# Optimization experiments

Measured on AMD Instinct MI355X. Metric: run time of the kernel, lower is better.

Reference implementation:

```python
import jax, jax.numpy as jnp
import numpy as np

B, C, W = 32, 128, 4096          # batch, channel (= emb_dim = D), window/input_dim
HID = [2048, 1024, 512]          # encoder hidden dims (last dim transforms)
K, D = 512, 128                  # codebook: K = hidden_dims[-1], D = emb_dim
BETA = 0.25


def setup_inputs() -> dict:
    key = jax.random.key(0)
    ks = jax.random.split(key, 12)
    def lin(k, fan_in, fan_out):
        return jax.random.normal(k, (fan_in, fan_out), jnp.float32) * (1.0 / np.sqrt(fan_in))
    inp = {"x": jax.random.normal(ks[0], (B, C, W), jnp.float32)}
    edims = [W] + HID  # 4096 -> 2048 -> 1024 -> 512
    for i in range(3):
        inp[f"ew{i}"] = lin(ks[1 + i], edims[i], edims[i + 1])
        inp[f"eb{i}"] = jnp.zeros((edims[i + 1],), jnp.float32)
    inp["codebook"] = jax.random.uniform(ks[4], (K, D), jnp.float32, -1.0 / K, 1.0 / K)
    ddims = [512, 1024, 2048, 4096]  # decoder mirrors encoder
    for i in range(3):
        inp[f"dw{i}"] = lin(ks[5 + i], ddims[i], ddims[i + 1])
        inp[f"db{i}"] = jnp.zeros((ddims[i + 1],), jnp.float32)
    return inp


def reference(x, ew0, eb0, ew1, eb1, ew2, eb2, codebook, dw0, db0, dw1, db1, dw2, db2):
    # ---- encoder: LinearBlock = Linear + ReLU over last dim ----
    h = x
    for wgt, b in ((ew0, eb0), (ew1, eb1), (ew2, eb2)):
        h = jax.nn.relu(h @ wgt + b)            # [B, C, L] with L shrinking to 512

    # ---- VectorQuantizer1d ----
    lat = jnp.swapaxes(h, 1, 2)                 # [B, L, D]
    flat = lat.reshape(-1, D)                   # [B*L, D]
    # cdist^2 via expansion, then argmin -> nearest-codebook lookup
    dist = (jnp.sum(flat * flat, axis=1, keepdims=True)
            + jnp.sum(codebook * codebook, axis=1)
            - 2.0 * flat @ codebook.T)          # [B*L, K]
    inds = jnp.argmin(dist, axis=1)             # [B*L]
    q = codebook[inds].reshape(lat.shape)       # one-hot matmul == gather

    commit = jnp.mean((jax.lax.stop_gradient(q) - lat) ** 2)
    embed = jnp.mean((q - jax.lax.stop_gradient(lat)) ** 2)
    vq_loss = BETA * commit + embed

    q_st = lat + jax.lax.stop_gradient(q - lat)  # straight-through estimator
    z = jnp.swapaxes(q_st, 1, 2)                 # back to [B, D, L]

    # ---- decoder: Linear+ReLU blocks, last block has no activation ----
    for i, (wgt, b) in enumerate(((dw0, db0), (dw1, db1), (dw2, db2))):
        z = z @ wgt + b
        if i < 2:
            z = jax.nn.relu(z)
    return z, x, vq_loss
```

## Files before the change

### kernel.cpp

```cpp
#include <hip/hip_runtime.h>


typedef _Float16 f16;
typedef _Float16 f16x8 __attribute__((ext_vector_type(8)));
typedef _Float16 f16x4 __attribute__((ext_vector_type(4)));
typedef float    f32x4 __attribute__((ext_vector_type(4)));

typedef const unsigned int __attribute__((address_space(1)))* gp1_t;
typedef unsigned int __attribute__((address_space(3)))*       lp3_t;

__device__ __forceinline__ void gl_lds16(const void* g, void* l) {
  __builtin_amdgcn_global_load_lds((gp1_t)g, (lp3_t)l, 16, 0, 0);
}

#define BATCH 32
#define CDIM  128
#define WDIM  4096
#define LDIM  512
#define KCB   512
#define DCB   128

#define SX    128.0f
#define SW    256.0f
#define SA    256.0f
#define SCB   4096.0f
#define SQ    4096.0f

#define BM 128
#define BN 128
#define BK 32

template<int SPLIT, int EPI>
__global__ __launch_bounds__(256, 2)
void vq_gemm(const f16* __restrict__ Ah, const f16* __restrict__ Al,
             const f16* __restrict__ Bh, const f16* __restrict__ Bl,
             const float* __restrict__ bias,
             void* __restrict__ Co, void* __restrict__ Co2,
             int M, int N, int K, float unscale, float outscale)
{
  __shared__ __align__(16) f16 sAh[BM * BK];
  __shared__ __align__(16) f16 sBh[BN * BK];
  __shared__ __align__(16) f16 sAl[SPLIT ? BM * BK : 8];
  __shared__ __align__(16) f16 sBl[SPLIT ? BN * BK : 8];

  const int tid  = threadIdx.x;
  const int lane = tid & 63;
  const int w    = tid >> 6;
  const int nb   = N / BN;
  const int bx   = blockIdx.x % nb;
  const int by   = blockIdx.x / nb;
  const int m0   = by * BM, n0 = bx * BN;
  const int wr   = w >> 1, wc = w & 1;
  const int fr   = lane & 15;
  const int ko   = (lane >> 4) * 8;

  f32x4 acc[4][4] = {};

  const int srow = lane >> 2;
  const int skb  = (lane & 3) * 8;

  for (int k0 = 0; k0 < K; k0 += BK) {
#pragma unroll
    for (int i = 0; i < 2; ++i) {
      const int c  = w * 2 + i;
      const size_t ga = (size_t)(m0 + c * 16 + srow) * K + k0 + skb;
      const size_t gb = (size_t)(n0 + c * 16 + srow) * K + k0 + skb;
      gl_lds16(Ah + ga, &sAh[c * 512]);
      gl_lds16(Bh + gb, &sBh[c * 512]);
      if (SPLIT) {
        gl_lds16(Al + ga, &sAl[c * 512]);
        gl_lds16(Bl + gb, &sBl[c * 512]);
      }
    }
    __syncthreads();

    f16x8 ah[4], bh[4], al[4], bl[4];
#pragma unroll
    for (int mi = 0; mi < 4; ++mi) {
      const int r = (wr * 64 + mi * 16 + fr) * BK + ko;
      ah[mi] = *(const f16x8*)&sAh[r];
      if (SPLIT) al[mi] = *(const f16x8*)&sAl[r];
    }
#pragma unroll
    for (int ni = 0; ni < 4; ++ni) {
      const int r = (wc * 64 + ni * 16 + fr) * BK + ko;
      bh[ni] = *(const f16x8*)&sBh[r];
      if (SPLIT) bl[ni] = *(const f16x8*)&sBl[r];
    }
#pragma unroll
    for (int mi = 0; mi < 4; ++mi)
#pragma unroll
      for (int ni = 0; ni < 4; ++ni) {
        acc[mi][ni] = __builtin_amdgcn_mfma_f32_16x16x32_f16(ah[mi], bh[ni], acc[mi][ni], 0, 0, 0);
        if (SPLIT) {
          acc[mi][ni] = __builtin_amdgcn_mfma_f32_16x16x32_f16(ah[mi], bl[ni], acc[mi][ni], 0, 0, 0);
          acc[mi][ni] = __builtin_amdgcn_mfma_f32_16x16x32_f16(al[mi], bh[ni], acc[mi][ni], 0, 0, 0);
        }
      }
    __syncthreads();
  }

  const int r4 = (lane >> 4) * 4;
#pragma unroll
  for (int mi = 0; mi < 4; ++mi) {
#pragma unroll
    for (int ni = 0; ni < 4; ++ni) {
      const int col = n0 + wc * 64 + ni * 16 + fr;
      const float bv = (EPI == 0) ? 0.0f : bias[col];
#pragma unroll
      for (int j = 0; j < 4; ++j) {
        const int row = m0 + wr * 64 + mi * 16 + r4 + j;
        float y = acc[mi][ni][j] * unscale;
        if (EPI != 0) y += bv;
        if (EPI == 1 || EPI == 2) y = fmaxf(y, 0.0f);
        const size_t idx = (size_t)row * N + col;
        if (EPI == 0 || EPI == 3) {
          ((float*)Co)[idx] = y;
        } else {
          const float ys = y * outscale;
          const f16 hi = (f16)ys;
          ((f16*)Co)[idx] = hi;
          if (EPI == 1) ((f16*)Co2)[idx] = (f16)(ys - (float)hi);
        }
      }
    }
  }
}

__global__ void vq_split(const float* __restrict__ in, f16* __restrict__ hi,
                         f16* __restrict__ lo, int n4, float scale)
{
  const int i = blockIdx.x * 256 + threadIdx.x;
  if (i >= n4) return;
  const float4 v = ((const float4*)in)[i];
  f16x4 h, l;
#pragma unroll
  for (int j = 0; j < 4; ++j) {
    const float s = (&v.x)[j] * scale;
    const f16 hh = (f16)s;
    h[j] = hh;
    l[j] = (f16)(s - (float)hh);
  }
  *(f16x4*)&hi[i * 4] = h;
  *(f16x4*)&lo[i * 4] = l;
}

template<int WRITE_LO>
__global__ void vq_tsplit(const float* __restrict__ W, f16* __restrict__ Th,
                          f16* __restrict__ Tl, int K, int N, float scale)
{
  __shared__ float t[32][33];
  const int n0 = blockIdx.x * 32, k0 = blockIdx.y * 32;
  const int tx = threadIdx.x & 31, ty = threadIdx.x >> 5;
#pragma unroll
  for (int i = 0; i < 4; ++i)
    t[ty + i * 8][tx] = W[(size_t)(k0 + ty + i * 8) * N + n0 + tx];
  __syncthreads();
#pragma unroll
  for (int i = 0; i < 4; ++i) {
    const int n = n0 + ty + i * 8;
    const float v = t[tx][ty + i * 8] * scale;
    const f16 hi = (f16)v;
    Th[(size_t)n * K + k0 + tx] = hi;
    if (WRITE_LO) Tl[(size_t)n * K + k0 + tx] = (f16)(v - (float)hi);
  }
}

__global__ void vq_tpose(const f16* __restrict__ Hh, const f16* __restrict__ Hl,
                         f16* __restrict__ Fh, f16* __restrict__ Fl)
{
  __shared__ f16 th[32][33];
  __shared__ f16 tl[32][33];
  const int bidx = blockIdx.x;
  const int b = bidx >> 6, rem = bidx & 63;
  const int l0 = (rem >> 2) * 32, c0 = (rem & 3) * 32;
  const int tx = threadIdx.x & 31, ty = threadIdx.x >> 5;
  const size_t hbase = (size_t)b * CDIM * LDIM;
#pragma unroll
  for (int i = 0; i < 4; ++i) {
    const int c = c0 + ty + i * 8;
    th[ty + i * 8][tx] = Hh[hbase + (size_t)c * LDIM + l0 + tx];
    tl[ty + i * 8][tx] = Hl[hbase + (size_t)c * LDIM + l0 + tx];
  }
  __syncthreads();
  const size_t fbase = (size_t)b * LDIM * DCB;
#pragma unroll
  for (int i = 0; i < 4; ++i) {
    const int l = l0 + ty + i * 8;
    Fh[fbase + (size_t)l * DCB + c0 + tx] = th[tx][ty + i * 8];
    Fl[fbase + (size_t)l * DCB + c0 + tx] = tl[tx][ty + i * 8];
  }
}

__global__ void vq_cbnorm(const float* __restrict__ cb, float* __restrict__ cbn)
{
  const int k = blockIdx.x * 256 + threadIdx.x;
  if (k >= KCB) return;
  float s = 0.f;
  for (int c = 0; c < DCB; ++c) { const float v = cb[k * DCB + c]; s += v * v; }
  cbn[k] = s;
}

__global__ void vq_argmin(const float* __restrict__ G, const float* __restrict__ cbn,
                          int* __restrict__ inds)
{
  const int row = blockIdx.x;
  const int lane = threadIdx.x;
  const float* g = G + (size_t)row * KCB;
  float best = 1e30f; int bi = 0;
#pragma unroll
  for (int j = 0; j < 8; ++j) {
    const int k = j * 64 + lane;
    const float d = cbn[k] - 2.0f * g[k];
    if (d < best) { best = d; bi = k; }
  }
  for (int off = 32; off; off >>= 1) {
    const float ov = __shfl_xor(best, off);
    const int oi = __shfl_xor(bi, off);
    if (ov < best || (ov == best && oi < bi)) { best = ov; bi = oi; }
  }
  if (lane == 0) inds[row] = bi;
}

__global__ void vq_gather(const float* __restrict__ cb, const int* __restrict__ inds,
                          f16* __restrict__ z0)
{
  const int t = blockIdx.x * 256 + threadIdx.x;
  const int l = t & 511, c = (t >> 9) & 127, b = t >> 16;
  const int ind = inds[b * LDIM + l];
  z0[t] = (f16)(cb[ind * DCB + c] * SQ);
}

__global__ void vq_loss(const f16* __restrict__ Fh, const f16* __restrict__ Fl,
                        const float* __restrict__ cb, const int* __restrict__ inds,
                        float* __restrict__ partials)
{
  const int gw = (blockIdx.x * 256 + threadIdx.x) >> 6;
  const int lane = threadIdx.x & 63;
  float s = 0.f;
  for (int r = gw; r < BATCH * LDIM; r += 1024) {
    const int ind = inds[r];
    const f16* fh = Fh + (size_t)r * DCB;
    const f16* fl = Fl + (size_t)r * DCB;
    const float* q = cb + (size_t)ind * DCB;
#pragma unroll
    for (int j = 0; j < 2; ++j) {
      const int c = j * 64 + lane;
      const float lat = ((float)fh[c] + (float)fl[c]) * (1.0f / SA);
      const float d = q[c] - lat;
      s += d * d;
    }
  }
  for (int off = 32; off; off >>= 1) s += __shfl_xor(s, off);
  __shared__ float wsum[4];
  if (lane == 0) wsum[threadIdx.x >> 6] = s;
  __syncthreads();
  if (threadIdx.x == 0) partials[blockIdx.x] = wsum[0] + wsum[1] + wsum[2] + wsum[3];
}

__global__ void vq_loss_final(const float* __restrict__ partials, float* __restrict__ out)
{
  float s = partials[threadIdx.x];
  for (int off = 32; off; off >>= 1) s += __shfl_xor(s, off);
  __shared__ float wsum[4];
  if ((threadIdx.x & 63) == 0) wsum[threadIdx.x >> 6] = s;
  __syncthreads();
  if (threadIdx.x == 0)
    out[0] = (wsum[0] + wsum[1] + wsum[2] + wsum[3]) * (1.25f / (float)(BATCH * LDIM * DCB));
}

extern "C" void kernel_launch(void* const* d_in, const int* in_sizes, int n_in,
                              void* d_out, int out_size, void* d_ws, size_t ws_size,
                              hipStream_t stream)
{
  const float* x   = (const float*)d_in[0];
  const float* ew0 = (const float*)d_in[1];
  const float* eb0 = (const float*)d_in[2];
  const float* ew1 = (const float*)d_in[3];
  const float* eb1 = (const float*)d_in[4];
  const float* ew2 = (const float*)d_in[5];
  const float* eb2 = (const float*)d_in[6];
  const float* cb  = (const float*)d_in[7];
  const float* dw0 = (const float*)d_in[8];
  const float* db0 = (const float*)d_in[9];
  const float* dw1 = (const float*)d_in[10];
  const float* db1 = (const float*)d_in[11];
  const float* dw2 = (const float*)d_in[12];
  const float* db2 = (const float*)d_in[13];
  float* out = (float*)d_out;

  constexpr size_t N_X  = 4096ull * 4096;
  constexpr size_t N_E0 = 4096ull * 2048, N_E1 = 2048ull * 1024, N_E2 = 1024ull * 512;
  constexpr size_t N_CB = 512ull * 128;
  constexpr size_t N_D0 = 512ull * 1024, N_D1 = 1024ull * 2048, N_D2 = 2048ull * 4096;
  constexpr size_t N_H0 = 4096ull * 2048, N_H1 = 4096ull * 1024, N_H2 = 4096ull * 512;
  constexpr size_t N_FL = 16384ull * 128;
  constexpr size_t N_Z1 = 4096ull * 1024;

  constexpr size_t O_EW0H = 0;
  constexpr size_t O_EW0L = O_EW0H + N_E0 * 2;
  constexpr size_t O_EW1H = O_EW0L + N_E0 * 2;
  constexpr size_t O_EW1L = O_EW1H + N_E1 * 2;
  constexpr size_t O_EW2H = O_EW1L + N_E1 * 2;
  constexpr size_t O_EW2L = O_EW2H + N_E2 * 2;
  constexpr size_t O_CBH  = O_EW2L + N_E2 * 2;
  constexpr size_t O_CBL  = O_CBH + N_CB * 2;
  constexpr size_t O_DW0  = O_CBL + N_CB * 2;
  constexpr size_t O_DW1  = O_DW0 + N_D0 * 2;
  constexpr size_t O_DW2  = O_DW1 + N_D1 * 2;
  constexpr size_t O_XH   = O_DW2 + N_D2 * 2;
  constexpr size_t O_XL   = O_XH + N_X * 2;
  constexpr size_t O_H0H  = O_XL + N_X * 2;
  constexpr size_t O_H0L  = O_H0H + N_H0 * 2;
  constexpr size_t O_H1H  = O_H0L + N_H0 * 2;
  constexpr size_t O_H1L  = O_H1H + N_H1 * 2;
  constexpr size_t O_H2H  = O_H1L + N_H1 * 2;
  constexpr size_t O_H2L  = O_H2H + N_H2 * 2;
  constexpr size_t O_FLH  = O_H2L + N_H2 * 2;
  constexpr size_t O_FLL  = O_FLH + N_FL * 2;
  constexpr size_t O_G    = O_XH;
  constexpr size_t O_INDS = O_XL;
  constexpr size_t O_CBN  = O_XL + (1ull << 17);
  constexpr size_t O_PART = O_XL + (1ull << 18);
  constexpr size_t O_Z0   = O_XL + (1ull << 20);
  constexpr size_t O_ZH1  = O_Z0 + N_H2 * 2;
  constexpr size_t O_ZH2  = O_ZH1 + N_Z1 * 2;

  char* ws = (char*)d_ws;
  f16*   XH = (f16*)(ws + O_XH);   f16* XL = (f16*)(ws + O_XL);
  f16* EW0H = (f16*)(ws + O_EW0H); f16* EW0L = (f16*)(ws + O_EW0L);
  f16* EW1H = (f16*)(ws + O_EW1H); f16* EW1L = (f16*)(ws + O_EW1L);
  f16* EW2H = (f16*)(ws + O_EW2H); f16* EW2L = (f16*)(ws + O_EW2L);
  f16*  CBH = (f16*)(ws + O_CBH);  f16* CBL = (f16*)(ws + O_CBL);
  f16*  DW0 = (f16*)(ws + O_DW0);  f16* DW1 = (f16*)(ws + O_DW1);  f16* DW2 = (f16*)(ws + O_DW2);
  f16*  H0H = (f16*)(ws + O_H0H);  f16* H0L = (f16*)(ws + O_H0L);
  f16*  H1H = (f16*)(ws + O_H1H);  f16* H1L = (f16*)(ws + O_H1L);
  f16*  H2H = (f16*)(ws + O_H2H);  f16* H2L = (f16*)(ws + O_H2L);
  f16*  FLH = (f16*)(ws + O_FLH);  f16* FLL = (f16*)(ws + O_FLL);
  float*  G = (float*)(ws + O_G);
  int* INDS = (int*)(ws + O_INDS);
  float* CBN = (float*)(ws + O_CBN);
  float* PART = (float*)(ws + O_PART);
  f16*   Z0 = (f16*)(ws + O_Z0);
  f16*  ZH1 = (f16*)(ws + O_ZH1);
  f16*  ZH2 = (f16*)(ws + O_ZH2);

  hipMemcpyAsync(out + 16777216, x, N_X * 4, hipMemcpyDeviceToDevice, stream);

  vq_split<<<(int)(N_X / 4 / 256), 256, 0, stream>>>(x, XH, XL, (int)(N_X / 4), SX);
  vq_split<<<(int)(N_CB / 4 / 256), 256, 0, stream>>>(cb, CBH, CBL, (int)(N_CB / 4), SCB);
  vq_tsplit<1><<<dim3(2048 / 32, 4096 / 32), 256, 0, stream>>>(ew0, EW0H, EW0L, 4096, 2048, SW);
  vq_tsplit<1><<<dim3(1024 / 32, 2048 / 32), 256, 0, stream>>>(ew1, EW1H, EW1L, 2048, 1024, SW);
  vq_tsplit<1><<<dim3(512 / 32, 1024 / 32), 256, 0, stream>>>(ew2, EW2H, EW2L, 1024, 512, SW);
  vq_tsplit<0><<<dim3(1024 / 32, 512 / 32), 256, 0, stream>>>(dw0, DW0, nullptr, 512, 1024, SW);
  vq_tsplit<0><<<dim3(2048 / 32, 1024 / 32), 256, 0, stream>>>(dw1, DW1, nullptr, 1024, 2048, SW);
  vq_tsplit<0><<<dim3(4096 / 32, 2048 / 32), 256, 0, stream>>>(dw2, DW2, nullptr, 2048, 4096, SW);

  vq_gemm<1, 1><<<(4096 / BM) * (2048 / BN), 256, 0, stream>>>(
      XH, XL, EW0H, EW0L, eb0, H0H, H0L, 4096, 2048, 4096, 1.0f / (SX * SW), SA);
  vq_gemm<1, 1><<<(4096 / BM) * (1024 / BN), 256, 0, stream>>>(
      H0H, H0L, EW1H, EW1L, eb1, H1H, H1L, 4096, 1024, 2048, 1.0f / (SA * SW), SA);
  vq_gemm<1, 1><<<(4096 / BM) * (512 / BN), 256, 0, stream>>>(
      H1H, H1L, EW2H, EW2L, eb2, H2H, H2L, 4096, 512, 1024, 1.0f / (SA * SW), SA);

  vq_tpose<<<BATCH * 64, 256, 0, stream>>>(H2H, H2L, FLH, FLL);
  vq_gemm<1, 0><<<(16384 / BM) * (512 / BN), 256, 0, stream>>>(
      FLH, FLL, CBH, CBL, nullptr, G, nullptr, 16384, 512, 128, 1.0f / (SA * SCB), 0.f);
  vq_cbnorm<<<2, 256, 0, stream>>>(cb, CBN);
  vq_argmin<<<16384, 64, 0, stream>>>(G, CBN, INDS);
  vq_gather<<<(BATCH * CDIM * LDIM) / 256, 256, 0, stream>>>(cb, INDS, Z0);
  vq_loss<<<256, 256, 0, stream>>>(FLH, FLL, cb, INDS, PART);
  vq_loss_final<<<1, 256, 0, stream>>>(PART, out + 33554432);

  vq_gemm<0, 2><<<(4096 / BM) * (1024 / BN), 256, 0, stream>>>(
      Z0, nullptr, DW0, nullptr, db0, ZH1, nullptr, 4096, 1024, 512, 1.0f / (SQ * SW), SQ);
  vq_gemm<0, 2><<<(4096 / BM) * (2048 / BN), 256, 0, stream>>>(
      ZH1, nullptr, DW1, nullptr, db1, ZH2, nullptr, 4096, 2048, 1024, 1.0f / (SQ * SW), SQ);
  vq_gemm<0, 3><<<(4096 / BM) * (4096 / BN), 256, 0, stream>>>(
      ZH2, nullptr, DW2, nullptr, db2, out, nullptr, 4096, 4096, 2048, 1.0f / (SQ * SW), 0.f);

  (void)in_sizes; (void)n_in; (void)out_size; (void)ws_size;
}
```

Before: 611.9 us.

## Add 8-wave 256x256 pipelined GEMM kernel for the three largest matmuls

Adds a new 512-thread GEMM kernel with 256x256 tiles, BK=64, XOR-swizzled LDS staged through global_load_lds, double buffering, explicit vmcnt and lgkmcnt waits, and s_setprio around the MFMA blocks. A grouped block-index swizzle is included for L2 reuse. The kernel replaces the 128x128 GEMM for the first encoder layer and the two largest decoder layers. The aim is more data reuse per tile and overlap of global loads with MFMA work. The hand-written wait counts and barriers are fragile, and the large per-block LDS footprint limits occupancy.

```diff
diff --git a/kernel.cpp b/kernel.cpp
--- a/kernel.cpp
+++ b/kernel.cpp
@@ -25,6 +25,170 @@
 #define SA    256.0f
 #define SCB   4096.0f
 #define SQ    4096.0f
+
+
+#define G8_SRC(t, As, Bs, kk) \
+  const f16 *As, *Bs; int kk; \
+  { int ts_ = (t) < NT ? (t) : NT - 1; int kg_ = ts_ << 6; \
+    if (SPLIT) { int sg_ = (kg_ >= 2 * K) ? 2 : ((kg_ >= K) ? 1 : 0); \
+      kk = kg_ - sg_ * K; As = (sg_ == 2) ? Al : Ah; Bs = (sg_ == 1) ? Bl : Bh; } \
+    else { As = Ah; Bs = Bh; kk = kg_; } }
+
+#define G8_STAGE(src, row0, kk, off) \
+  _Pragma("unroll") \
+  for (int j_ = 0; j_ < 2; ++j_) { \
+    const int p_ = j_ * 8192 + tid * 16; \
+    const int r_ = p_ >> 7; \
+    const int c_ = (p_ >> 4) & 7; \
+    gl_lds16((src) + (size_t)((row0) + r_) * K + (kk) + ((c_ ^ (r_ & 7)) << 3), \
+             smem + (off) + p_); \
+  }
+
+#define G8_STAGE_A(t, u) do { G8_SRC(t, As_, Bs_, kk_) \
+  G8_STAGE(As_, m0 + (u) * 128, kk_, ((t) & 1) * ASZ + (u) * 16384) } while (0)
+#define G8_STAGE_B(t, u) do { G8_SRC(t, As_, Bs_, kk_) \
+  G8_STAGE(Bs_, n0 + (u) * 128, kk_, BBASE + ((t) & 1) * BSZ + (u) * 16384) } while (0)
+
+#define G8_READ_A(buf, mh) \
+  _Pragma("unroll") \
+  for (int m_ = 0; m_ < MR2; ++m_) { \
+    const int r_ = wr * (MR * 16) + ((mh) * MR2 + m_) * 16 + fr; \
+    _Pragma("unroll") \
+    for (int ks_ = 0; ks_ < 2; ++ks_) \
+      ar[m_][ks_] = *(const f16x8*)(smem + (buf) * ASZ + r_ * 128 + \
+                                    ((((ks_ << 2) + hq) ^ (r_ & 7)) << 4)); \
+  }
+
+#define G8_READ_B(buf, nh, br) \
+  _Pragma("unroll") \
+  for (int n_ = 0; n_ < 2; ++n_) { \
+    const int r_ = wc * 64 + ((nh) * 2 + n_) * 16 + fr; \
+    _Pragma("unroll") \
+    for (int ks_ = 0; ks_ < 2; ++ks_) \
+      br[n_][ks_] = *(const f16x8*)(smem + BBASE + (buf) * BSZ + r_ * 128 + \
+                                    ((((ks_ << 2) + hq) ^ (r_ & 7)) << 4)); \
+  }
+
+#define G8_MFMA(mh, nh, br) \
+  _Pragma("unroll") \
+  for (int m_ = 0; m_ < MR2; ++m_) \
+  _Pragma("unroll") \
+  for (int n_ = 0; n_ < 2; ++n_) \
+  _Pragma("unroll") \
+  for (int ks_ = 0; ks_ < 2; ++ks_) \
+    acc[(mh) * MR2 + m_][(nh) * 2 + n_] = __builtin_amdgcn_mfma_f32_16x16x32_f16( \
+        ar[m_][ks_], br[n_][ks_], acc[(mh) * MR2 + m_][(nh) * 2 + n_], 0, 0, 0);
+
+#define G8_BAR() do { asm volatile("" ::: "memory"); \
+  __builtin_amdgcn_s_barrier(); asm volatile("" ::: "memory"); } while (0)
+#define G8_LGKM0() do { asm volatile("s_waitcnt lgkmcnt(0)" ::: "memory"); \
+  __builtin_amdgcn_sched_barrier(0); } while (0)
+#define G8_VMGATE() do { \
+  if constexpr (BUNITS == 2) asm volatile("s_waitcnt vmcnt(4)" ::: "memory"); \
+  else                       asm volatile("s_waitcnt vmcnt(2)" ::: "memory"); } while (0)
+#define G8_PRIO1() __builtin_amdgcn_s_setprio(1)
+#define G8_PRIO0() __builtin_amdgcn_s_setprio(0)
+
+template<int SPLIT, int EPI, int WM, int WN, int MR>
+__global__ __launch_bounds__(512, 2)
+void vq_gemm8(const f16* __restrict__ Ah, const f16* __restrict__ Al,
+              const f16* __restrict__ Bh, const f16* __restrict__ Bl,
+              const float* __restrict__ bias,
+              void* __restrict__ Co, void* __restrict__ Co2,
+              int M, int N, int K, float unscale, float outscale)
+{
+  constexpr int MR2 = MR / 2;
+  constexpr int GBM = WM * MR * 16;
+  constexpr int GBN = WN * 64;
+  constexpr int BUNITS = GBN / 128;
+  constexpr int ASZ = GBM * 128;
+  constexpr int BSZ = GBN * 128;
+  constexpr int BBASE = 2 * ASZ;
+  constexpr int LDSZ = 2 * ASZ + 2 * BSZ;
+
+  __shared__ __align__(16) char smem[LDSZ];
+
+  const int tid = threadIdx.x;
+  const int lane = tid & 63;
+  const int w = tid >> 6;
+  const int wr = w / WN, wc = w % WN;
+  const int fr = lane & 15, hq = lane >> 4;
+
+  const int nbx = N / GBN;
+  const int cpx = gridDim.x >> 3;
+  const int swz = ((int)blockIdx.x & 7) * cpx + ((int)blockIdx.x >> 3);
+  const int bx = swz % nbx, by = swz / nbx;
+  const int m0 = by * GBM, n0 = bx * GBN;
+
+  const int NT = (SPLIT ? 3 * K : K) >> 6;
+  const int NI = NT >> 1;
+
+  f32x4 acc[MR][4] = {};
+  f16x8 ar[MR2][2], br0[2][2], br1[2][2];
+
+  G8_STAGE_B(0, 0); if constexpr (BUNITS == 2) G8_STAGE_B(0, 1);
+  G8_STAGE_A(0, 0); G8_STAGE_A(0, 1);
+  G8_STAGE_B(1, 0); if constexpr (BUNITS == 2) G8_STAGE_B(1, 1);
+
+  for (int i = 0; i < NI; ++i) {
+    const int to = 2 * i + 1, te = 2 * i + 2, to2 = 2 * i + 3;
+    G8_VMGATE(); G8_BAR();
+    G8_READ_A(0, 0) G8_READ_B(0, 0, br0)
+    G8_STAGE_A(to, 0);
+    G8_BAR(); G8_LGKM0(); G8_PRIO1(); G8_MFMA(0, 0, br0) G8_PRIO0();
+    G8_BAR();
+    G8_READ_B(0, 1, br1)
+    G8_STAGE_A(to, 1);
+    G8_BAR(); G8_LGKM0(); G8_PRIO1(); G8_MFMA(0, 1, br1) G8_PRIO0();
+    G8_BAR();
+    G8_READ_A(0, 1)
+    G8_STAGE_B(te, 0);
+    G8_BAR(); G8_LGKM0(); G8_PRIO1(); G8_MFMA(1, 0, br0) G8_PRIO0();
+    G8_BAR();
+    if constexpr (BUNITS == 2) G8_STAGE_B(te, 1);
+    G8_BAR(); G8_PRIO1(); G8_MFMA(1, 1, br1) G8_PRIO0();
+    G8_VMGATE(); G8_BAR();
+    G8_READ_A(1, 0) G8_READ_B(1, 0, br0)
+    G8_STAGE_A(te, 0);
+    G8_BAR(); G8_LGKM0(); G8_PRIO1(); G8_MFMA(0, 0, br0) G8_PRIO0();
+    G8_BAR();
+    G8_READ_B(1, 1, br1)
+    G8_STAGE_A(te, 1);
+    G8_BAR(); G8_LGKM0(); G8_PRIO1(); G8_MFMA(0, 1, br1) G8_PRIO0();
+    G8_BAR();
+    G8_READ_A(1, 1)
+    G8_STAGE_B(to2, 0);
+    G8_BAR(); G8_LGKM0(); G8_PRIO1(); G8_MFMA(1, 0, br0) G8_PRIO0();
+    G8_BAR();
+    if constexpr (BUNITS == 2) G8_STAGE_B(to2, 1);
+    G8_BAR(); G8_PRIO1(); G8_MFMA(1, 1, br1) G8_PRIO0();
+  }
+
+  const int r4 = hq * 4;
+#pragma unroll
+  for (int mi = 0; mi < MR; ++mi) {
+#pragma unroll
+    for (int ni = 0; ni < 4; ++ni) {
+      const int col = n0 + wc * 64 + ni * 16 + fr;
+      const float bv = (EPI == 0) ? 0.f : bias[col];
+#pragma unroll
+      for (int j = 0; j < 4; ++j) {
+        const int row = m0 + wr * (MR * 16) + mi * 16 + r4 + j;
+        float y = acc[mi][ni][j] * unscale;
+        if (EPI != 0) y += bv;
+        if (EPI == 1 || EPI == 2) y = fmaxf(y, 0.f);
+        const size_t idx = (size_t)row * N + col;
+        if (EPI == 0 || EPI == 3) ((float*)Co)[idx] = y;
+        else {
+          const float ys = y * outscale;
+          const f16 hv = (f16)ys;
+          ((f16*)Co)[idx] = hv;
+          if (EPI == 1) ((f16*)Co2)[idx] = (f16)(ys - (float)hv);
+        }
+      }
+    }
+  }
+}
 
 #define BM 128
 #define BN 128
@@ -118,9 +282,9 @@
           ((float*)Co)[idx] = y;
         } else {
           const float ys = y * outscale;
-          const f16 hi = (f16)ys;
-          ((f16*)Co)[idx] = hi;
-          if (EPI == 1) ((f16*)Co2)[idx] = (f16)(ys - (float)hi);
+          const f16 hv = (f16)ys;
+          ((f16*)Co)[idx] = hv;
+          if (EPI == 1) ((f16*)Co2)[idx] = (f16)(ys - (float)hv);
         }
       }
     }
@@ -160,9 +324,9 @@
   for (int i = 0; i < 4; ++i) {
     const int n = n0 + ty + i * 8;
     const float v = t[tx][ty + i * 8] * scale;
-    const f16 hi = (f16)v;
-    Th[(size_t)n * K + k0 + tx] = hi;
-    if (WRITE_LO) Tl[(size_t)n * K + k0 + tx] = (f16)(v - (float)hi);
+    const f16 hv = (f16)v;
+    Th[(size_t)n * K + k0 + tx] = hv;
+    if (WRITE_LO) Tl[(size_t)n * K + k0 + tx] = (f16)(v - (float)hv);
   }
 }
 
@@ -356,7 +520,7 @@
   vq_tsplit<0><<<dim3(2048 / 32, 1024 / 32), 256, 0, stream>>>(dw1, DW1, nullptr, 1024, 2048, SW);
   vq_tsplit<0><<<dim3(4096 / 32, 2048 / 32), 256, 0, stream>>>(dw2, DW2, nullptr, 2048, 4096, SW);
 
-  vq_gemm<1, 1><<<(4096 / BM) * (2048 / BN), 256, 0, stream>>>(
+  vq_gemm8<1, 1, 4, 2, 4><<<256, 512, 0, stream>>>(
       XH, XL, EW0H, EW0L, eb0, H0H, H0L, 4096, 2048, 4096, 1.0f / (SX * SW), SA);
   vq_gemm<1, 1><<<(4096 / BM) * (1024 / BN), 256, 0, stream>>>(
       H0H, H0L, EW1H, EW1L, eb1, H1H, H1L, 4096, 1024, 2048, 1.0f / (SA * SW), SA);
@@ -374,9 +538,9 @@
 
   vq_gemm<0, 2><<<(4096 / BM) * (1024 / BN), 256, 0, stream>>>(
       Z0, nullptr, DW0, nullptr, db0, ZH1, nullptr, 4096, 1024, 512, 1.0f / (SQ * SW), SQ);
-  vq_gemm<0, 2><<<(4096 / BM) * (2048 / BN), 256, 0, stream>>>(
+  vq_gemm8<0, 2, 4, 2, 4><<<256, 512, 0, stream>>>(
       ZH1, nullptr, DW1, nullptr, db1, ZH2, nullptr, 4096, 2048, 1024, 1.0f / (SQ * SW), SQ);
-  vq_gemm<0, 3><<<(4096 / BM) * (4096 / BN), 256, 0, stream>>>(
+  vq_gemm8<0, 3, 2, 4, 8><<<256, 512, 0, stream>>>(
       ZH2, nullptr, DW2, nullptr, db2, out, nullptr, 4096, 4096, 2048, 1.0f / (SQ * SW), 0.f);
 
   (void)in_sizes; (void)n_in; (void)out_size; (void)ws_size;
```

After: 565.2 us. 7.6% less time.
